# Performance work log

Measured on AMD Instinct MI355X. Metric: run time of the kernel, lower is better.

Reference implementation:

```python
import jax, jax.numpy as jnp
import numpy as np

HEAD = 16
EPS = 1.1920929e-07  # torch.finfo(float32).eps, used by nn.RMSNorm when eps=None


def _rms(x, g):
    return x * jax.lax.rsqrt(jnp.mean(x * x, axis=-1, keepdims=True) + EPS) * g


def _heads(t):
    b, L, dm = t.shape
    return t.reshape(b, L, HEAD, dm // HEAD).transpose(0, 2, 1, 3)  # b h L d


def setup_inputs() -> dict:
    key = jax.random.key(0)
    ks = jax.random.split(key, 8)
    b, L, dims = 1, 1024, 1024
    s = dims ** -0.5
    x = jax.random.normal(ks[0], (b, L, dims), jnp.float32)
    pt = jax.random.normal(ks[1], (b, L, dims), jnp.float32)
    # additive causal mask (finite large-negative to stay grad-safe)
    mask = jnp.triu(jnp.full((L, L), -1e9, jnp.float32), k=1)
    return {
        "x": x, "pt": pt, "mask": mask,
        "gq": jnp.ones((dims,), jnp.float32),
        "Wq": jax.random.normal(ks[2], (dims, dims), jnp.float32) * s,
        "bq": jnp.zeros((dims,), jnp.float32),
        "gkv": jnp.ones((dims,), jnp.float32),
        "Wkv": jax.random.normal(ks[3], (dims, 2 * dims), jnp.float32) * s,
        "bkv": jnp.zeros((2 * dims,), jnp.float32),
        "gc": jnp.ones((dims,), jnp.float32),
        "Wc": jax.random.normal(ks[4], (dims, dims), jnp.float32) * s,
        "bc": jnp.zeros((dims,), jnp.float32),
        "Wout": jax.random.normal(ks[5], (dims, dims), jnp.float32) * s,
        "bout": jnp.zeros((dims,), jnp.float32),
        "context_window": 16,
    }


def reference(x, pt, mask, gq, Wq, bq, gkv, Wkv, bkv, gc, Wc, bc, Wout, bout, context_window):
    b, L, dims = x.shape
    d = dims // HEAD
    q = _heads(_rms(x, gq) @ Wq + bq)                      # b h L d
    kv = (_rms(x, gkv) @ Wkv + bkv).reshape(b, L, 2, HEAD, d)
    k = kv[:, :, 0].transpose(0, 2, 1, 3)                  # b h L d
    v = kv[:, :, 1].transpose(0, 2, 1, 3)
    c = _heads(_rms(pt, gc) @ Wc + bc)                     # b h L d

    # triplet_scores[i,j] = sum_{t=max(0,min(i,j)-w)}^{min(L,max(i,j)+w)-1} q_i . (k_j * c_t)
    # Vectorize with prefix sums over c: window sum = P[end] - P[start],
    # where end depends only on max(i,j) and start only on min(i,j).
    P = jnp.concatenate([jnp.zeros((b, HEAD, 1, d), x.dtype), jnp.cumsum(c, axis=2)], axis=2)  # b h L+1 d
    idx = jnp.arange(L)
    S = jnp.clip(idx - context_window, 0, L)   # start for min-index
    E = jnp.clip(idx + context_window, 0, L)   # end for max-index
    PE = jnp.take(P, E, axis=2)                # b h L d
    PS = jnp.take(P, S, axis=2)

    U = jnp.einsum('bhid,bhjd->bhij', q, k * PE)        # end from j (i<=j branch)
    V = jnp.einsum('bhid,bhjd->bhij', q * PS, k)        # start from i (i<=j branch)
    U2 = jnp.einsum('bhid,bhjd->bhij', q * PE, k)       # end from i (i>j branch)
    V2 = jnp.einsum('bhid,bhjd->bhij', q, k * PS)       # start from j (i>j branch)
    lower = idx[:, None] <= idx[None, :]
    triplet = jnp.where(lower, U - V, U2 - V2)          # b h L L

    scale = d ** -0.5
    qk = jnp.einsum('bhid,bhjd->bhij', q, k) * scale + triplet + mask[:L, :L]
    attn = jax.nn.softmax(qk, axis=-1)
    wv = jnp.einsum('bhij,bhjd->bhid', attn, v)
    out = wv.transpose(0, 2, 1, 3).reshape(b, L, dims) @ Wout + bout  # dropout p=0.01 is identity at eval
    return out
```

## Files before the change

kernel.cpp:

```cpp
#include <hip/hip_runtime.h>

#define LQ 1024
#define DM 1024


typedef __attribute__((ext_vector_type(8))) short bf16x8;
typedef __attribute__((ext_vector_type(4))) float f32x4;

#define MFMA(a, b, c) __builtin_amdgcn_mfma_f32_16x16x32_bf16((a), (b), (c), 0, 0, 0)
#define WAIT_LDS() __builtin_amdgcn_s_waitcnt(0xC07F)

__device__ __forceinline__ unsigned short f2bf(float x) {
    unsigned int u = __float_as_uint(x);
    return (unsigned short)((u + 0x7FFFu + ((u >> 16) & 1u)) >> 16);
}
__device__ __forceinline__ float bf2f(unsigned short h) {
    return __uint_as_float(((unsigned int)h) << 16);
}
__device__ __forceinline__ void gload16(const void* gp, void* lp) {
    __builtin_amdgcn_global_load_lds(
        (const __attribute__((address_space(1))) void*)gp,
        (__attribute__((address_space(3))) void*)lp, 16, 0, 0);
}
__device__ __forceinline__ void store_split4(unsigned short* ph, unsigned short* pl,
                                             float4 v) {
    unsigned short h0 = f2bf(v.x), h1 = f2bf(v.y), h2 = f2bf(v.z), h3 = f2bf(v.w);
    uint2 a;
    a.x = (unsigned)h0 | ((unsigned)h1 << 16);
    a.y = (unsigned)h2 | ((unsigned)h3 << 16);
    *(uint2*)ph = a;
    unsigned short l0 = f2bf(v.x - bf2f(h0)), l1 = f2bf(v.y - bf2f(h1));
    unsigned short l2 = f2bf(v.z - bf2f(h2)), l3 = f2bf(v.w - bf2f(h3));
    uint2 b;
    b.x = (unsigned)l0 | ((unsigned)l1 << 16);
    b.y = (unsigned)l2 | ((unsigned)l3 << 16);
    *(uint2*)pl = b;
}

__device__ __forceinline__ void rms_body(
    int row, const float* __restrict__ x, const float* __restrict__ pt,
    const float* __restrict__ gq, const float* __restrict__ gkv,
    const float* __restrict__ gc,
    unsigned short* xqn_h, unsigned short* xqn_l,
    unsigned short* xkvn_h, unsigned short* xkvn_l,
    unsigned short* ptn_h, unsigned short* ptn_l)
{
    const int t = threadIdx.x;
    const bool isx = row < LQ;
    const float* src = isx ? (x + (size_t)row * DM)
                           : (pt + (size_t)(row - LQ) * DM);
    float4 v = ((const float4*)src)[t];
    float ss = v.x*v.x + v.y*v.y + v.z*v.z + v.w*v.w;
    #pragma unroll
    for (int o = 32; o > 0; o >>= 1) ss += __shfl_down(ss, o);
    __shared__ float red[4];
    if ((t & 63) == 0) red[t >> 6] = ss;
    __syncthreads();
    const float r = rsqrtf((red[0] + red[1] + red[2] + red[3]) * (1.0f / DM)
                           + 1.1920929e-07f);
    const size_t base = (size_t)(isx ? row : row - LQ) * DM + t * 4;
    if (isx) {
        float4 g1 = ((const float4*)gq)[t];
        float4 g2 = ((const float4*)gkv)[t];
        float4 y1, y2;
        y1.x = v.x*r*g1.x; y1.y = v.y*r*g1.y; y1.z = v.z*r*g1.z; y1.w = v.w*r*g1.w;
        y2.x = v.x*r*g2.x; y2.y = v.y*r*g2.y; y2.z = v.z*r*g2.z; y2.w = v.w*r*g2.w;
        store_split4(xqn_h + base, xqn_l + base, y1);
        store_split4(xkvn_h + base, xkvn_l + base, y2);
    } else {
        float4 g = ((const float4*)gc)[t];
        float4 y;
        y.x = v.x*r*g.x; y.y = v.y*r*g.y; y.z = v.z*r*g.z; y.w = v.w*r*g.w;
        store_split4(ptn_h + base, ptn_l + base, y);
    }
}

__device__ __forceinline__ void wsplit_body(
    const float* __restrict__ in, unsigned short* oh, unsigned short* ol,
    int K, int N, int bx, int by)
{
    __shared__ float T[64 * 65];
    const int t = threadIdx.x;
    const int tx = t & 15, ty = t >> 4;
    const int c0 = bx * 64, r0 = by * 64;
    #pragma unroll
    for (int p = 0; p < 4; ++p) {
        int row = ty + p * 16;
        float4 v = *(const float4*)(in + (size_t)(r0 + row) * N + c0 + tx * 4);
        T[row * 65 + tx * 4 + 0] = v.x;
        T[row * 65 + tx * 4 + 1] = v.y;
        T[row * 65 + tx * 4 + 2] = v.z;
        T[row * 65 + tx * 4 + 3] = v.w;
    }
    __syncthreads();
    #pragma unroll
    for (int p = 0; p < 4; ++p) {
        int n = ty + p * 16;
        float4 w;
        w.x = T[(tx * 4 + 0) * 65 + n];
        w.y = T[(tx * 4 + 1) * 65 + n];
        w.z = T[(tx * 4 + 2) * 65 + n];
        w.w = T[(tx * 4 + 3) * 65 + n];
        size_t o = (size_t)(c0 + n) * K + r0 + tx * 4;
        store_split4(oh + o, ol + o, w);
    }
}

__global__ __launch_bounds__(256) void prep_kernel(
    const float* __restrict__ x, const float* __restrict__ pt,
    const float* __restrict__ gq, const float* __restrict__ gkv,
    const float* __restrict__ gc,
    const float* __restrict__ Wq, const float* __restrict__ Wkv,
    const float* __restrict__ Wc, const float* __restrict__ Wout,
    unsigned short* xqn_h, unsigned short* xqn_l,
    unsigned short* xkvn_h, unsigned short* xkvn_l,
    unsigned short* ptn_h, unsigned short* ptn_l,
    unsigned short* WqT_h, unsigned short* WqT_l,
    unsigned short* WkvT_h, unsigned short* WkvT_l,
    unsigned short* WcT_h, unsigned short* WcT_l,
    unsigned short* WoT_h, unsigned short* WoT_l)
{
    const int b = blockIdx.x;
    if (b < 2048) {
        rms_body(b, x, pt, gq, gkv, gc, xqn_h, xqn_l, xkvn_h, xkvn_l, ptn_h, ptn_l);
    } else if (b < 2304) {
        int s = b - 2048; wsplit_body(Wq, WqT_h, WqT_l, 1024, 1024, s & 15, s >> 4);
    } else if (b < 2816) {
        int s = b - 2304; wsplit_body(Wkv, WkvT_h, WkvT_l, 1024, 2048, s & 31, s >> 5);
    } else if (b < 3072) {
        int s = b - 2816; wsplit_body(Wc, WcT_h, WcT_l, 1024, 1024, s & 15, s >> 4);
    } else {
        int s = b - 3072; wsplit_body(Wout, WoT_h, WoT_l, 1024, 1024, s & 15, s >> 4);
    }
}

__device__ __forceinline__ void gemm3p(
    const unsigned short* __restrict__ Ah, const unsigned short* __restrict__ Al,
    const unsigned short* __restrict__ Bh, const unsigned short* __restrict__ Bl,
    const float* __restrict__ bias, float* __restrict__ out, int N, int mt, int nt)
{
    __shared__ unsigned short sAh[128 * 32], sAl[128 * 32];
    __shared__ unsigned short sBh[64 * 32], sBl[64 * 32];
    const int t = threadIdx.x;
    const int lane = t & 63, w = t >> 6;
    const int wm = w >> 1, wn = w & 1;
    const int n16 = lane & 15, quad = lane >> 4;
    const int srow = t >> 2, scol = (t & 3) * 8;
    f32x4 zero = {0.f, 0.f, 0.f, 0.f};
    f32x4 acc[4][2];
    #pragma unroll
    for (int ms = 0; ms < 4; ++ms)
        #pragma unroll
        for (int ns = 0; ns < 2; ++ns) acc[ms][ns] = zero;

    for (int kt = 0; kt < 32; ++kt) {
        const int k0 = kt * 32;
        __syncthreads();
        #pragma unroll
        for (int p = 0; p < 2; ++p) {
            const size_t ga = (size_t)(mt * 128 + srow + p * 64) * 1024 + k0 + scol;
            const int lb = w * 512 + p * 2048;
            gload16(Ah + ga, sAh + lb);
            gload16(Al + ga, sAl + lb);
        }
        {
            const size_t gb = (size_t)(nt * 64 + srow) * 1024 + k0 + scol;
            gload16(Bh + gb, sBh + w * 512);
            gload16(Bl + gb, sBl + w * 512);
        }
        __syncthreads();
        bf16x8 afh[4], afl[4], bfh[2], bfl[2];
        #pragma unroll
        for (int ms = 0; ms < 4; ++ms) {
            int r = wm * 64 + ms * 16 + n16;
            afh[ms] = *(const bf16x8*)&sAh[r * 32 + quad * 8];
            afl[ms] = *(const bf16x8*)&sAl[r * 32 + quad * 8];
        }
        #pragma unroll
        for (int ns = 0; ns < 2; ++ns) {
            int r = wn * 32 + ns * 16 + n16;
            bfh[ns] = *(const bf16x8*)&sBh[r * 32 + quad * 8];
            bfl[ns] = *(const bf16x8*)&sBl[r * 32 + quad * 8];
        }
        #pragma unroll
        for (int ms = 0; ms < 4; ++ms)
            #pragma unroll
            for (int ns = 0; ns < 2; ++ns) {
                acc[ms][ns] = MFMA(afh[ms], bfh[ns], acc[ms][ns]);
                acc[ms][ns] = MFMA(afh[ms], bfl[ns], acc[ms][ns]);
                acc[ms][ns] = MFMA(afl[ms], bfh[ns], acc[ms][ns]);
            }
    }
    #pragma unroll
    for (int ns = 0; ns < 2; ++ns) {
        const int col = nt * 64 + wn * 32 + ns * 16 + n16;
        const float bv = bias[col];
        #pragma unroll
        for (int ms = 0; ms < 4; ++ms) {
            const int row0 = mt * 128 + wm * 64 + ms * 16 + quad * 4;
            #pragma unroll
            for (int reg = 0; reg < 4; ++reg)
                out[(size_t)(row0 + reg) * N + col] = acc[ms][ns][reg] + bv;
        }
    }
}

__global__ __launch_bounds__(256) void proj_kernel(
    const unsigned short* __restrict__ xqn_h, const unsigned short* __restrict__ xqn_l,
    const unsigned short* __restrict__ xkvn_h, const unsigned short* __restrict__ xkvn_l,
    const unsigned short* __restrict__ ptn_h, const unsigned short* __restrict__ ptn_l,
    const unsigned short* __restrict__ WqT_h, const unsigned short* __restrict__ WqT_l,
    const unsigned short* __restrict__ WkvT_h, const unsigned short* __restrict__ WkvT_l,
    const unsigned short* __restrict__ WcT_h, const unsigned short* __restrict__ WcT_l,
    const float* __restrict__ bq, const float* __restrict__ bkv,
    const float* __restrict__ bc,
    float* __restrict__ Qb, float* __restrict__ KVb, float* __restrict__ Cb)
{
    const int bid = blockIdx.x;
    if (bid < 128) {
        gemm3p(xqn_h, xqn_l, WqT_h, WqT_l, bq, Qb, 1024, bid >> 4, bid & 15);
    } else if (bid < 384) {
        int b2 = bid - 128;
        gemm3p(xkvn_h, xkvn_l, WkvT_h, WkvT_l, bkv, KVb, 2048, b2 >> 5, b2 & 31);
    } else {
        int b2 = bid - 384;
        gemm3p(ptn_h, ptn_l, WcT_h, WcT_l, bc, Cb, 1024, b2 >> 4, b2 & 15);
    }
}

__global__ __launch_bounds__(256) void csum_kernel(const float* __restrict__ Cb,
                                                   float* __restrict__ csum)
{
    const int cid = blockIdx.x >> 2;
    const int col = ((blockIdx.x & 3) << 8) + threadIdx.x;
    const float* p = Cb + (size_t)cid * 32 * 1024 + col;
    float s = 0.f;
    #pragma unroll 8
    for (int r = 0; r < 32; ++r) s += p[(size_t)r * 1024];
    csum[cid * 1024 + col] = s;
}

__global__ __launch_bounds__(256) void scanp_kernel(const float* __restrict__ Cb,
                                                    const float* __restrict__ csum,
                                                    float* __restrict__ Pb)
{
    const int cid = blockIdx.x >> 2;
    const int col = ((blockIdx.x & 3) << 8) + threadIdx.x;
    float run = 0.f;
    for (int c = 0; c < cid; ++c) run += csum[c * 1024 + col];
    const float* p = Cb + (size_t)cid * 32 * 1024 + col;
    float* q = Pb + (size_t)cid * 32 * 1024 + col;
    for (int r = 0; r < 32; ++r) {
        q[(size_t)r * 1024] = run;
        run += p[(size_t)r * 1024];
    }
    if (cid == 31) Pb[(size_t)1024 * 1024 + col] = run;
}

__global__ __launch_bounds__(256) void abv_kernel(
    const float* __restrict__ Qb, const float* __restrict__ KVb,
    const float* __restrict__ Pb, const int* __restrict__ cwp,
    unsigned short* __restrict__ Aah, unsigned short* __restrict__ Aal,
    unsigned short* __restrict__ Bah, unsigned short* __restrict__ Bal,
    unsigned short* __restrict__ VT)
{
    const int b = blockIdx.x;
    if (b < 4096) {
        const int gid = b * 256 + threadIdx.x;
        const int i = gid >> 10;
        const int col = gid & 1023;
        const int h = col >> 6, dd = col & 63;
        const int cw = *cwp;
        const int E = min(i + cw, LQ);
        const int S = max(i - cw, 0);
        const float pe = Pb[(size_t)E * 1024 + col];
        const float ps = Pb[(size_t)S * 1024 + col];
        const float q = Qb[gid];
        const float k = KVb[(size_t)i * 2048 + col];
        const float scale = 0.125f;
        const size_t base = ((size_t)(h * 1024 + i)) * 128;
        float a0 = q, a1 = q * pe;
        float b0 = k * (scale - ps), b1 = k;
        unsigned short hv;
        hv = f2bf(a0); Aah[base + dd] = hv;      Aal[base + dd] = f2bf(a0 - bf2f(hv));
        hv = f2bf(a1); Aah[base + 64 + dd] = hv; Aal[base + 64 + dd] = f2bf(a1 - bf2f(hv));
        hv = f2bf(b0); Bah[base + dd] = hv;      Bal[base + dd] = f2bf(b0 - bf2f(hv));
        hv = f2bf(b1); Bah[base + 64 + dd] = hv; Bal[base + 64 + dd] = f2bf(b1 - bf2f(hv));
    } else {
        const int s = b - 4096;
        const int h = s >> 4, j0 = (s & 15) * 64;
        __shared__ float T[64 * 65];
        const int t = threadIdx.x;
        const int tx = t & 15, ty = t >> 4;
        #pragma unroll
        for (int p = 0; p < 4; ++p) {
            int j = ty + p * 16;
            float4 v = *(const float4*)(KVb + (size_t)(j0 + j) * 2048 + 1024 + h * 64 + tx * 4);
            T[j * 65 + tx * 4 + 0] = v.x;
            T[j * 65 + tx * 4 + 1] = v.y;
            T[j * 65 + tx * 4 + 2] = v.z;
            T[j * 65 + tx * 4 + 3] = v.w;
        }
        __syncthreads();
        #pragma unroll
        for (int p = 0; p < 4; ++p) {
            int d = ty + p * 16;
            unsigned short e0 = f2bf(T[(tx * 4 + 0) * 65 + d]);
            unsigned short e1 = f2bf(T[(tx * 4 + 1) * 65 + d]);
            unsigned short e2 = f2bf(T[(tx * 4 + 2) * 65 + d]);
            unsigned short e3 = f2bf(T[(tx * 4 + 3) * 65 + d]);
            uint2 pk;
            pk.x = (unsigned)e0 | ((unsigned)e1 << 16);
            pk.y = (unsigned)e2 | ((unsigned)e3 << 16);
            *(uint2*)(VT + (size_t)(h * 64 + d) * 1024 + j0 + tx * 4) = pk;
        }
    }
}

__global__ __launch_bounds__(256, 4) void attn_kernel(
    const unsigned short* __restrict__ Aah, const unsigned short* __restrict__ Aal,
    const unsigned short* __restrict__ Bah, const unsigned short* __restrict__ Bal,
    const unsigned short* __restrict__ VT,
    unsigned short* __restrict__ wvh, unsigned short* __restrict__ wvl)
{
    __shared__ unsigned short PsAll[4][16 * 68];
    __shared__ float cO[4][16 * 68];
    __shared__ float cM[4][16], cL[4][16];

    const int t = threadIdx.x;
    const int lane = t & 63, wid = t >> 6;
    unsigned short* Ps = PsAll[wid];
    const int b = blockIdx.x;
    const int h = b & 15;
    const int q = (b >> 4) & 15;
    const int group = b >> 8;
    const int it16 = (group == 0) ? q : (group == 1) ? (31 - q)
                   : (group == 2) ? (32 + q) : (63 - q);
    const int i0 = it16 * 16;
    const int njt = (i0 >> 6) + 1;
    const int n16 = lane & 15, quad = lane >> 4;

    bf16x8 afh[4], afl[4];
    {
        const size_t ar = ((size_t)(h * 1024 + i0 + n16)) * 128 + quad * 8;
        #pragma unroll
        for (int kc = 0; kc < 4; ++kc) {
            afh[kc] = *(const bf16x8*)(Aah + ar + kc * 32);
            afl[kc] = *(const bf16x8*)(Aal + ar + kc * 32);
        }
    }

    f32x4 zero = {0.f, 0.f, 0.f, 0.f};
    f32x4 oacc[4];
    #pragma unroll
    for (int dt = 0; dt < 4; ++dt) oacc[dt] = zero;
    float mrow[4], lrow[4];
    #pragma unroll
    for (int reg = 0; reg < 4; ++reg) { mrow[reg] = -1e30f; lrow[reg] = 0.f; }

    for (int jt = wid; jt < njt; jt += 4) {
        const int j0 = jt * 64;
        f32x4 s[4];
        #pragma unroll
        for (int jj = 0; jj < 4; ++jj) s[jj] = zero;
        #pragma unroll
        for (int jj = 0; jj < 4; ++jj) {
            const size_t br = ((size_t)(h * 1024 + j0 + jj * 16 + n16)) * 128 + quad * 8;
            #pragma unroll
            for (int kc = 0; kc < 4; ++kc) {
                bf16x8 bh = *(const bf16x8*)(Bah + br + kc * 32);
                bf16x8 bl = *(const bf16x8*)(Bal + br + kc * 32);
                s[jj] = MFMA(afh[kc], bh, s[jj]);
                s[jj] = MFMA(afh[kc], bl, s[jj]);
                s[jj] = MFMA(afl[kc], bh, s[jj]);
            }
        }
        if (jt == njt - 1) {
            const int ibase = i0 + quad * 4;
            #pragma unroll
            for (int jj = 0; jj < 4; ++jj) {
                const int j = j0 + jj * 16 + n16;
                #pragma unroll
                for (int reg = 0; reg < 4; ++reg)
                    if (j > ibase + reg) s[jj][reg] = -1e30f;
            }
        }

        float alpha[4];
        #pragma unroll
        for (int reg = 0; reg < 4; ++reg) {
            float mt_ = fmaxf(fmaxf(s[0][reg], s[1][reg]), fmaxf(s[2][reg], s[3][reg]));
            mt_ = fmaxf(mt_, __shfl_xor(mt_, 1));
            mt_ = fmaxf(mt_, __shfl_xor(mt_, 2));
            mt_ = fmaxf(mt_, __shfl_xor(mt_, 4));
            mt_ = fmaxf(mt_, __shfl_xor(mt_, 8));
            const float mn = fmaxf(mrow[reg], mt_);
            alpha[reg] = __expf(mrow[reg] - mn);
            mrow[reg] = mn;
            float rs = 0.f;
            #pragma unroll
            for (int jj = 0; jj < 4; ++jj) {
                float p = __expf(s[jj][reg] - mn);
                s[jj][reg] = p;
                rs += p;
            }
            rs += __shfl_xor(rs, 1); rs += __shfl_xor(rs, 2);
            rs += __shfl_xor(rs, 4); rs += __shfl_xor(rs, 8);
            lrow[reg] = lrow[reg] * alpha[reg] + rs;
        }

        WAIT_LDS();
        #pragma unroll
        for (int jj = 0; jj < 4; ++jj)
            #pragma unroll
            for (int reg = 0; reg < 4; ++reg)
                Ps[(quad * 4 + reg) * 68 + jj * 16 + n16] = f2bf(s[jj][reg]);
        WAIT_LDS();
        bf16x8 pf0 = *(const bf16x8*)&Ps[n16 * 68 + quad * 8];
        bf16x8 pf1 = *(const bf16x8*)&Ps[n16 * 68 + 32 + quad * 8];

        #pragma unroll
        for (int dt = 0; dt < 4; ++dt) {
            #pragma unroll
            for (int reg = 0; reg < 4; ++reg) oacc[dt][reg] *= alpha[reg];
            const size_t vr = ((size_t)(h * 64 + dt * 16 + n16)) * 1024 + j0 + quad * 8;
            bf16x8 vf0 = *(const bf16x8*)(VT + vr);
            bf16x8 vf1 = *(const bf16x8*)(VT + vr + 32);
            oacc[dt] = MFMA(pf0, vf0, oacc[dt]);
            oacc[dt] = MFMA(pf1, vf1, oacc[dt]);
        }
    }

    #pragma unroll
    for (int dt = 0; dt < 4; ++dt)
        #pragma unroll
        for (int reg = 0; reg < 4; ++reg)
            cO[wid][(quad * 4 + reg) * 68 + dt * 16 + n16] = oacc[dt][reg];
    if (n16 == 0) {
        #pragma unroll
        for (int reg = 0; reg < 4; ++reg) {
            cM[wid][quad * 4 + reg] = mrow[reg];
            cL[wid][quad * 4 + reg] = lrow[reg];
        }
    }
    __syncthreads();
    #pragma unroll
    for (int u = 0; u < 4; ++u) {
        const int p = u * 256 + t;
        const int r = p >> 6, d = p & 63;
        const float m0 = cM[0][r], m1 = cM[1][r], m2 = cM[2][r], m3 = cM[3][r];
        const float M = fmaxf(fmaxf(m0, m1), fmaxf(m2, m3));
        const float e0 = __expf(m0 - M), e1 = __expf(m1 - M);
        const float e2 = __expf(m2 - M), e3 = __expf(m3 - M);
        const float L = e0 * cL[0][r] + e1 * cL[1][r] + e2 * cL[2][r] + e3 * cL[3][r];
        const float o = e0 * cO[0][r * 68 + d] + e1 * cO[1][r * 68 + d]
                      + e2 * cO[2][r * 68 + d] + e3 * cO[3][r * 68 + d];
        const float v = o / L;
        const size_t oi = (size_t)(i0 + r) * 1024 + h * 64 + d;
        const unsigned short hv = f2bf(v);
        wvh[oi] = hv;
        wvl[oi] = f2bf(v - bf2f(hv));
    }
}

__global__ __launch_bounds__(128) void outgemm_kernel(
    const unsigned short* __restrict__ Ah, const unsigned short* __restrict__ Al,
    const unsigned short* __restrict__ Bh, const unsigned short* __restrict__ Bl,
    const float* __restrict__ bias, float* __restrict__ out)
{
    __shared__ unsigned short sAh[64 * 32], sAl[64 * 32];
    __shared__ unsigned short sBh[32 * 32], sBl[32 * 32];
    const int t = threadIdx.x;
    const int lane = t & 63, w = t >> 6;
    const int n16 = lane & 15, quad = lane >> 4;
    const int mt = blockIdx.x >> 5, nt = blockIdx.x & 31;
    const int srow = t >> 2, scol = (t & 3) * 8;
    f32x4 zero = {0.f, 0.f, 0.f, 0.f};
    f32x4 acc[2][2];
    #pragma unroll
    for (int ms = 0; ms < 2; ++ms)
        #pragma unroll
        for (int ns = 0; ns < 2; ++ns) acc[ms][ns] = zero;

    for (int kt = 0; kt < 32; ++kt) {
        const int k0 = kt * 32;
        __syncthreads();
        #pragma unroll
        for (int p = 0; p < 2; ++p) {
            const size_t ga = (size_t)(mt * 64 + srow + p * 32) * 1024 + k0 + scol;
            const int lb = w * 512 + p * 1024;
            gload16(Ah + ga, sAh + lb);
            gload16(Al + ga, sAl + lb);
        }
        {
            const size_t gb = (size_t)(nt * 32 + srow) * 1024 + k0 + scol;
            gload16(Bh + gb, sBh + w * 512);
            gload16(Bl + gb, sBl + w * 512);
        }
        __syncthreads();
        bf16x8 ah[2], al[2], bh[2], bl[2];
        #pragma unroll
        for (int ms = 0; ms < 2; ++ms) {
            int r = w * 32 + ms * 16 + n16;
            ah[ms] = *(const bf16x8*)&sAh[r * 32 + quad * 8];
            al[ms] = *(const bf16x8*)&sAl[r * 32 + quad * 8];
        }
        #pragma unroll
        for (int ns = 0; ns < 2; ++ns) {
            int r = ns * 16 + n16;
            bh[ns] = *(const bf16x8*)&sBh[r * 32 + quad * 8];
            bl[ns] = *(const bf16x8*)&sBl[r * 32 + quad * 8];
        }
        #pragma unroll
        for (int ms = 0; ms < 2; ++ms)
            #pragma unroll
            for (int ns = 0; ns < 2; ++ns) {
                acc[ms][ns] = MFMA(ah[ms], bh[ns], acc[ms][ns]);
                acc[ms][ns] = MFMA(ah[ms], bl[ns], acc[ms][ns]);
                acc[ms][ns] = MFMA(al[ms], bh[ns], acc[ms][ns]);
            }
    }
    #pragma unroll
    for (int ns = 0; ns < 2; ++ns) {
        const int col = nt * 32 + ns * 16 + n16;
        const float bv = bias[col];
        #pragma unroll
        for (int ms = 0; ms < 2; ++ms) {
            const int row0 = mt * 64 + w * 32 + ms * 16 + quad * 4;
            #pragma unroll
            for (int reg = 0; reg < 4; ++reg)
                out[(size_t)(row0 + reg) * 1024 + col] = acc[ms][ns][reg] + bv;
        }
    }
}

extern "C" void kernel_launch(void* const* d_in, const int* in_sizes, int n_in,
                              void* d_out, int out_size, void* d_ws, size_t ws_size,
                              hipStream_t stream) {
    (void)in_sizes; (void)n_in; (void)out_size; (void)ws_size;
    const float* x    = (const float*)d_in[0];
    const float* pt   = (const float*)d_in[1];
    const float* gq   = (const float*)d_in[3];
    const float* Wq   = (const float*)d_in[4];
    const float* bq   = (const float*)d_in[5];
    const float* gkv  = (const float*)d_in[6];
    const float* Wkv  = (const float*)d_in[7];
    const float* bkv  = (const float*)d_in[8];
    const float* gc   = (const float*)d_in[9];
    const float* Wc   = (const float*)d_in[10];
    const float* bc   = (const float*)d_in[11];
    const float* Wout = (const float*)d_in[12];
    const float* bout = (const float*)d_in[13];
    const int*   cw   = (const int*)d_in[14];
    float* out = (float*)d_out;

    char* W = (char*)d_ws;
    const size_t MB = 1u << 20;
    #define US(off) ((unsigned short*)(W + (size_t)(off)))
    #define FP(off) ((float*)(W + (size_t)(off)))
    unsigned short* xqn_h  = US(0 * MB);
    unsigned short* xqn_l  = US(2 * MB);
    unsigned short* xkvn_h = US(4 * MB);
    unsigned short* xkvn_l = US(6 * MB);
    unsigned short* ptn_h  = US(8 * MB);
    unsigned short* ptn_l  = US(10 * MB);
    unsigned short* WqT_h  = US(12 * MB);
    unsigned short* WqT_l  = US(14 * MB);
    unsigned short* WkvT_h = US(16 * MB);
    unsigned short* WkvT_l = US(20 * MB);
    unsigned short* WcT_h  = US(24 * MB);
    unsigned short* WcT_l  = US(26 * MB);
    unsigned short* WoT_h  = US(28 * MB);
    unsigned short* WoT_l  = US(30 * MB);
    float* Qb   = FP(32 * MB);
    float* KVb  = FP(36 * MB);
    float* Cb   = FP(44 * MB);
    float* Pb   = FP(48 * MB);
    float* csum = FP(52 * MB + 256 * 1024);
    unsigned short* Aah = US(0 * MB);
    unsigned short* Aal = US(4 * MB);
    unsigned short* Bah = US(8 * MB);
    unsigned short* Bal = US(12 * MB);
    unsigned short* VTb = US(16 * MB);
    unsigned short* wv_h = US(18 * MB);
    unsigned short* wv_l = US(20 * MB);
    #undef US
    #undef FP

    hipLaunchKernelGGL(prep_kernel, dim3(3328), dim3(256), 0, stream,
                       x, pt, gq, gkv, gc, Wq, Wkv, Wc, Wout,
                       xqn_h, xqn_l, xkvn_h, xkvn_l, ptn_h, ptn_l,
                       WqT_h, WqT_l, WkvT_h, WkvT_l, WcT_h, WcT_l, WoT_h, WoT_l);
    hipLaunchKernelGGL(proj_kernel, dim3(512), dim3(256), 0, stream,
                       xqn_h, xqn_l, xkvn_h, xkvn_l, ptn_h, ptn_l,
                       WqT_h, WqT_l, WkvT_h, WkvT_l, WcT_h, WcT_l,
                       bq, bkv, bc, Qb, KVb, Cb);
    hipLaunchKernelGGL(csum_kernel, dim3(128), dim3(256), 0, stream, Cb, csum);
    hipLaunchKernelGGL(scanp_kernel, dim3(128), dim3(256), 0, stream, Cb, csum, Pb);
    hipLaunchKernelGGL(abv_kernel, dim3(4352), dim3(256), 0, stream,
                       Qb, KVb, Pb, cw, Aah, Aal, Bah, Bal, VTb);
    hipLaunchKernelGGL(attn_kernel, dim3(1024), dim3(256), 0, stream,
                       Aah, Aal, Bah, Bal, VTb, wv_h, wv_l);
    hipLaunchKernelGGL(outgemm_kernel, dim3(512), dim3(128), 0, stream,
                       wv_h, wv_l, WoT_h, WoT_l, bout, out);
}
```

Baseline: 225.3 us.

## Process two 16-row query tiles per 512-thread attention block, prefetch V earlier

The attention kernel now uses 512-thread blocks that each cover 32 query rows: pairs of waves share a key tile index, with each wave of a pair handling one 16-row half. Because the two halves read the same K/V tiles, those tiles can be reused through cache. The grid halves to 512 blocks, and block ordering pairs early and late rows to balance causal work. V fragments are now loaded right after the score MFMAs so their latency overlaps the softmax. The final combine reduces over the four waves belonging to each half. In exchange, register pressure and LDS use per block go up, and the coarser blocks could reduce occupancy or load balance.

New measurement: 239.2 us. 6.2% more time.

```diff
diff --git a/kernel.cpp b/kernel.cpp
--- a/kernel.cpp
+++ b/kernel.cpp
@@ -317,27 +317,27 @@
     }
 }
 
-__global__ __launch_bounds__(256, 4) void attn_kernel(
+__global__ __launch_bounds__(512, 4) void attn_kernel(
     const unsigned short* __restrict__ Aah, const unsigned short* __restrict__ Aal,
     const unsigned short* __restrict__ Bah, const unsigned short* __restrict__ Bal,
     const unsigned short* __restrict__ VT,
     unsigned short* __restrict__ wvh, unsigned short* __restrict__ wvl)
 {
-    __shared__ unsigned short PsAll[4][16 * 68];
-    __shared__ float cO[4][16 * 68];
-    __shared__ float cM[4][16], cL[4][16];
+    __shared__ unsigned short PsAll[8][16 * 68];
+    __shared__ float cO[8][16 * 68];
+    __shared__ float cM[8][16], cL[8][16];
 
     const int t = threadIdx.x;
     const int lane = t & 63, wid = t >> 6;
+    const int jp = wid >> 1, isub = wid & 1;
     unsigned short* Ps = PsAll[wid];
     const int b = blockIdx.x;
     const int h = b & 15;
-    const int q = (b >> 4) & 15;
-    const int group = b >> 8;
-    const int it16 = (group == 0) ? q : (group == 1) ? (31 - q)
-                   : (group == 2) ? (32 + q) : (63 - q);
-    const int i0 = it16 * 16;
-    const int njt = (i0 >> 6) + 1;
+    const int q4 = (b >> 4) & 15;
+    const int it32 = (b >> 8) ? (31 - q4) : q4;
+    const int i0b = it32 * 32;
+    const int i0 = i0b + isub * 16;
+    const int njt = (it32 >> 1) + 1;
     const int n16 = lane & 15, quad = lane >> 4;
 
     bf16x8 afh[4], afl[4];
@@ -358,7 +358,7 @@
     #pragma unroll
     for (int reg = 0; reg < 4; ++reg) { mrow[reg] = -1e30f; lrow[reg] = 0.f; }
 
-    for (int jt = wid; jt < njt; jt += 4) {
+    for (int jt = jp; jt < njt; jt += 4) {
         const int j0 = jt * 64;
         f32x4 s[4];
         #pragma unroll
@@ -375,6 +375,15 @@
                 s[jj] = MFMA(afl[kc], bh, s[jj]);
             }
         }
+
+        bf16x8 vf[4][2];
+        #pragma unroll
+        for (int dt = 0; dt < 4; ++dt) {
+            const size_t vr = ((size_t)(h * 64 + dt * 16 + n16)) * 1024 + j0 + quad * 8;
+            vf[dt][0] = *(const bf16x8*)(VT + vr);
+            vf[dt][1] = *(const bf16x8*)(VT + vr + 32);
+        }
+
         if (jt == njt - 1) {
             const int ibase = i0 + quad * 4;
             #pragma unroll
@@ -423,11 +432,8 @@
         for (int dt = 0; dt < 4; ++dt) {
             #pragma unroll
             for (int reg = 0; reg < 4; ++reg) oacc[dt][reg] *= alpha[reg];
-            const size_t vr = ((size_t)(h * 64 + dt * 16 + n16)) * 1024 + j0 + quad * 8;
-            bf16x8 vf0 = *(const bf16x8*)(VT + vr);
-            bf16x8 vf1 = *(const bf16x8*)(VT + vr + 32);
-            oacc[dt] = MFMA(pf0, vf0, oacc[dt]);
-            oacc[dt] = MFMA(pf1, vf1, oacc[dt]);
+            oacc[dt] = MFMA(pf0, vf[dt][0], oacc[dt]);
+            oacc[dt] = MFMA(pf1, vf[dt][1], oacc[dt]);
         }
     }
 
@@ -446,17 +452,20 @@
     __syncthreads();
     #pragma unroll
     for (int u = 0; u < 4; ++u) {
-        const int p = u * 256 + t;
-        const int r = p >> 6, d = p & 63;
-        const float m0 = cM[0][r], m1 = cM[1][r], m2 = cM[2][r], m3 = cM[3][r];
+        const int p = u * 512 + t;
+        const int s = p >> 10;
+        const int rem = p & 1023;
+        const int r = rem >> 6, d = rem & 63;
+        const int w0 = s, w1 = s + 2, w2 = s + 4, w3 = s + 6;
+        const float m0 = cM[w0][r], m1 = cM[w1][r], m2 = cM[w2][r], m3 = cM[w3][r];
         const float M = fmaxf(fmaxf(m0, m1), fmaxf(m2, m3));
         const float e0 = __expf(m0 - M), e1 = __expf(m1 - M);
         const float e2 = __expf(m2 - M), e3 = __expf(m3 - M);
-        const float L = e0 * cL[0][r] + e1 * cL[1][r] + e2 * cL[2][r] + e3 * cL[3][r];
-        const float o = e0 * cO[0][r * 68 + d] + e1 * cO[1][r * 68 + d]
-                      + e2 * cO[2][r * 68 + d] + e3 * cO[3][r * 68 + d];
+        const float L = e0 * cL[w0][r] + e1 * cL[w1][r] + e2 * cL[w2][r] + e3 * cL[w3][r];
+        const float o = e0 * cO[w0][r * 68 + d] + e1 * cO[w1][r * 68 + d]
+                      + e2 * cO[w2][r * 68 + d] + e3 * cO[w3][r * 68 + d];
         const float v = o / L;
-        const size_t oi = (size_t)(i0 + r) * 1024 + h * 64 + d;
+        const size_t oi = (size_t)(i0b + s * 16 + r) * 1024 + h * 64 + d;
         const unsigned short hv = f2bf(v);
         wvh[oi] = hv;
         wvl[oi] = f2bf(v - bf2f(hv));
@@ -599,7 +608,7 @@
     hipLaunchKernelGGL(scanp_kernel, dim3(128), dim3(256), 0, stream, Cb, csum, Pb);
     hipLaunchKernelGGL(abv_kernel, dim3(4352), dim3(256), 0, stream,
                        Qb, KVb, Pb, cw, Aah, Aal, Bah, Bal, VTb);
-    hipLaunchKernelGGL(attn_kernel, dim3(1024), dim3(256), 0, stream,
+    hipLaunchKernelGGL(attn_kernel, dim3(512), dim3(512), 0, stream,
                        Aah, Aal, Bah, Bal, VTb, wv_h, wv_l);
     hipLaunchKernelGGL(outgemm_kernel, dim3(512), dim3(128), 0, stream,
                        wv_h, wv_l, WoT_h, WoT_l, bout, out);
```

## Enlarge GEMM tiles to 128x128 and 64x64, reload Q fragments per tile

Applied to the files above, without the earlier changes.

The projection GEMM moves from 128x64 tiles with 256 threads to 128x128 tiles with 512 threads (8 waves as 2x4). The output GEMM moves from 64x32 tiles with 128 threads to 64x64 tiles with 256 threads (2x2 waves). Both halve the grid and cut redundant global loads of the shared operand. The attention kernel now loads the A fragments inside the j-tile loop instead of once before it, which lowers register pressure but adds repeated global reads. The larger blocks also mean fewer blocks in flight on the device.

Measured after the change: 234.2 us. 1.04x slower.

```diff
diff --git a/kernel.cpp b/kernel.cpp
--- a/kernel.cpp
+++ b/kernel.cpp
@@ -140,10 +140,10 @@
     const float* __restrict__ bias, float* __restrict__ out, int N, int mt, int nt)
 {
     __shared__ unsigned short sAh[128 * 32], sAl[128 * 32];
-    __shared__ unsigned short sBh[64 * 32], sBl[64 * 32];
+    __shared__ unsigned short sBh[128 * 32], sBl[128 * 32];
     const int t = threadIdx.x;
     const int lane = t & 63, w = t >> 6;
-    const int wm = w >> 1, wn = w & 1;
+    const int wm = w >> 2, wn = w & 3;
     const int n16 = lane & 15, quad = lane >> 4;
     const int srow = t >> 2, scol = (t & 3) * 8;
     f32x4 zero = {0.f, 0.f, 0.f, 0.f};
@@ -155,19 +155,13 @@
 
     for (int kt = 0; kt < 32; ++kt) {
         const int k0 = kt * 32;
+        const size_t ga = (size_t)(mt * 128 + srow) * 1024 + k0 + scol;
+        const size_t gb = (size_t)(nt * 128 + srow) * 1024 + k0 + scol;
         __syncthreads();
-        #pragma unroll
-        for (int p = 0; p < 2; ++p) {
-            const size_t ga = (size_t)(mt * 128 + srow + p * 64) * 1024 + k0 + scol;
-            const int lb = w * 512 + p * 2048;
-            gload16(Ah + ga, sAh + lb);
-            gload16(Al + ga, sAl + lb);
-        }
-        {
-            const size_t gb = (size_t)(nt * 64 + srow) * 1024 + k0 + scol;
-            gload16(Bh + gb, sBh + w * 512);
-            gload16(Bl + gb, sBl + w * 512);
-        }
+        gload16(Ah + ga, sAh + w * 512);
+        gload16(Al + ga, sAl + w * 512);
+        gload16(Bh + gb, sBh + w * 512);
+        gload16(Bl + gb, sBl + w * 512);
         __syncthreads();
         bf16x8 afh[4], afl[4], bfh[2], bfl[2];
         #pragma unroll
@@ -193,7 +187,7 @@
     }
     #pragma unroll
     for (int ns = 0; ns < 2; ++ns) {
-        const int col = nt * 64 + wn * 32 + ns * 16 + n16;
+        const int col = nt * 128 + wn * 32 + ns * 16 + n16;
         const float bv = bias[col];
         #pragma unroll
         for (int ms = 0; ms < 4; ++ms) {
@@ -205,7 +199,7 @@
     }
 }
 
-__global__ __launch_bounds__(256) void proj_kernel(
+__global__ __launch_bounds__(512) void proj_kernel(
     const unsigned short* __restrict__ xqn_h, const unsigned short* __restrict__ xqn_l,
     const unsigned short* __restrict__ xkvn_h, const unsigned short* __restrict__ xkvn_l,
     const unsigned short* __restrict__ ptn_h, const unsigned short* __restrict__ ptn_l,
@@ -217,14 +211,14 @@
     float* __restrict__ Qb, float* __restrict__ KVb, float* __restrict__ Cb)
 {
     const int bid = blockIdx.x;
-    if (bid < 128) {
-        gemm3p(xqn_h, xqn_l, WqT_h, WqT_l, bq, Qb, 1024, bid >> 4, bid & 15);
-    } else if (bid < 384) {
-        int b2 = bid - 128;
-        gemm3p(xkvn_h, xkvn_l, WkvT_h, WkvT_l, bkv, KVb, 2048, b2 >> 5, b2 & 31);
+    if (bid < 64) {
+        gemm3p(xqn_h, xqn_l, WqT_h, WqT_l, bq, Qb, 1024, bid >> 3, bid & 7);
+    } else if (bid < 192) {
+        int b2 = bid - 64;
+        gemm3p(xkvn_h, xkvn_l, WkvT_h, WkvT_l, bkv, KVb, 2048, b2 >> 4, b2 & 15);
     } else {
-        int b2 = bid - 384;
-        gemm3p(ptn_h, ptn_l, WcT_h, WcT_l, bc, Cb, 1024, b2 >> 4, b2 & 15);
+        int b2 = bid - 192;
+        gemm3p(ptn_h, ptn_l, WcT_h, WcT_l, bc, Cb, 1024, b2 >> 3, b2 & 7);
     }
 }
 
@@ -340,26 +334,24 @@
     const int njt = (i0 >> 6) + 1;
     const int n16 = lane & 15, quad = lane >> 4;
 
-    bf16x8 afh[4], afl[4];
-    {
-        const size_t ar = ((size_t)(h * 1024 + i0 + n16)) * 128 + quad * 8;
+    f32x4 zero = {0.f, 0.f, 0.f, 0.f};
+    f32x4 oacc[4];
+    #pragma unroll
+    for (int dt = 0; dt < 4; ++dt) oacc[dt] = zero;
+    float mrow[4], lrow[4];
+    #pragma unroll
+    for (int reg = 0; reg < 4; ++reg) { mrow[reg] = -1e30f; lrow[reg] = 0.f; }
+
+    const size_t ar = ((size_t)(h * 1024 + i0 + n16)) * 128 + quad * 8;
+
+    for (int jt = wid; jt < njt; jt += 4) {
+        const int j0 = jt * 64;
+        bf16x8 afh[4], afl[4];
         #pragma unroll
         for (int kc = 0; kc < 4; ++kc) {
             afh[kc] = *(const bf16x8*)(Aah + ar + kc * 32);
             afl[kc] = *(const bf16x8*)(Aal + ar + kc * 32);
         }
-    }
-
-    f32x4 zero = {0.f, 0.f, 0.f, 0.f};
-    f32x4 oacc[4];
-    #pragma unroll
-    for (int dt = 0; dt < 4; ++dt) oacc[dt] = zero;
-    float mrow[4], lrow[4];
-    #pragma unroll
-    for (int reg = 0; reg < 4; ++reg) { mrow[reg] = -1e30f; lrow[reg] = 0.f; }
-
-    for (int jt = wid; jt < njt; jt += 4) {
-        const int j0 = jt * 64;
         f32x4 s[4];
         #pragma unroll
         for (int jj = 0; jj < 4; ++jj) s[jj] = zero;
@@ -463,17 +455,18 @@
     }
 }
 
-__global__ __launch_bounds__(128) void outgemm_kernel(
+__global__ __launch_bounds__(256) void outgemm_kernel(
     const unsigned short* __restrict__ Ah, const unsigned short* __restrict__ Al,
     const unsigned short* __restrict__ Bh, const unsigned short* __restrict__ Bl,
     const float* __restrict__ bias, float* __restrict__ out)
 {
     __shared__ unsigned short sAh[64 * 32], sAl[64 * 32];
-    __shared__ unsigned short sBh[32 * 32], sBl[32 * 32];
+    __shared__ unsigned short sBh[64 * 32], sBl[64 * 32];
     const int t = threadIdx.x;
     const int lane = t & 63, w = t >> 6;
+    const int wm = w >> 1, wn = w & 1;
     const int n16 = lane & 15, quad = lane >> 4;
-    const int mt = blockIdx.x >> 5, nt = blockIdx.x & 31;
+    const int mt = blockIdx.x >> 4, nt = blockIdx.x & 15;
     const int srow = t >> 2, scol = (t & 3) * 8;
     f32x4 zero = {0.f, 0.f, 0.f, 0.f};
     f32x4 acc[2][2];
@@ -484,30 +477,24 @@
 
     for (int kt = 0; kt < 32; ++kt) {
         const int k0 = kt * 32;
+        const size_t ga = (size_t)(mt * 64 + srow) * 1024 + k0 + scol;
+        const size_t gb = (size_t)(nt * 64 + srow) * 1024 + k0 + scol;
         __syncthreads();
-        #pragma unroll
-        for (int p = 0; p < 2; ++p) {
-            const size_t ga = (size_t)(mt * 64 + srow + p * 32) * 1024 + k0 + scol;
-            const int lb = w * 512 + p * 1024;
-            gload16(Ah + ga, sAh + lb);
-            gload16(Al + ga, sAl + lb);
-        }
-        {
-            const size_t gb = (size_t)(nt * 32 + srow) * 1024 + k0 + scol;
-            gload16(Bh + gb, sBh + w * 512);
-            gload16(Bl + gb, sBl + w * 512);
-        }
+        gload16(Ah + ga, sAh + w * 512);
+        gload16(Al + ga, sAl + w * 512);
+        gload16(Bh + gb, sBh + w * 512);
+        gload16(Bl + gb, sBl + w * 512);
         __syncthreads();
         bf16x8 ah[2], al[2], bh[2], bl[2];
         #pragma unroll
         for (int ms = 0; ms < 2; ++ms) {
-            int r = w * 32 + ms * 16 + n16;
+            int r = wm * 32 + ms * 16 + n16;
             ah[ms] = *(const bf16x8*)&sAh[r * 32 + quad * 8];
             al[ms] = *(const bf16x8*)&sAl[r * 32 + quad * 8];
         }
         #pragma unroll
         for (int ns = 0; ns < 2; ++ns) {
-            int r = ns * 16 + n16;
+            int r = wn * 32 + ns * 16 + n16;
             bh[ns] = *(const bf16x8*)&sBh[r * 32 + quad * 8];
             bl[ns] = *(const bf16x8*)&sBl[r * 32 + quad * 8];
         }
@@ -522,11 +509,11 @@
     }
     #pragma unroll
     for (int ns = 0; ns < 2; ++ns) {
-        const int col = nt * 32 + ns * 16 + n16;
+        const int col = nt * 64 + wn * 32 + ns * 16 + n16;
         const float bv = bias[col];
         #pragma unroll
         for (int ms = 0; ms < 2; ++ms) {
-            const int row0 = mt * 64 + w * 32 + ms * 16 + quad * 4;
+            const int row0 = mt * 64 + wm * 32 + ms * 16 + quad * 4;
             #pragma unroll
             for (int reg = 0; reg < 4; ++reg)
                 out[(size_t)(row0 + reg) * 1024 + col] = acc[ms][ns][reg] + bv;
@@ -591,7 +578,7 @@
                        x, pt, gq, gkv, gc, Wq, Wkv, Wc, Wout,
                        xqn_h, xqn_l, xkvn_h, xkvn_l, ptn_h, ptn_l,
                        WqT_h, WqT_l, WkvT_h, WkvT_l, WcT_h, WcT_l, WoT_h, WoT_l);
-    hipLaunchKernelGGL(proj_kernel, dim3(512), dim3(256), 0, stream,
+    hipLaunchKernelGGL(proj_kernel, dim3(256), dim3(512), 0, stream,
                        xqn_h, xqn_l, xkvn_h, xkvn_l, ptn_h, ptn_l,
                        WqT_h, WqT_l, WkvT_h, WkvT_l, WcT_h, WcT_l,
                        bq, bkv, bc, Qb, KVb, Cb);
@@ -601,6 +588,6 @@
                        Qb, KVb, Pb, cw, Aah, Aal, Bah, Bal, VTb);
     hipLaunchKernelGGL(attn_kernel, dim3(1024), dim3(256), 0, stream,
                        Aah, Aal, Bah, Bal, VTb, wv_h, wv_l);
-    hipLaunchKernelGGL(outgemm_kernel, dim3(512), dim3(128), 0, stream,
+    hipLaunchKernelGGL(outgemm_kernel, dim3(256), dim3(256), 0, stream,
                        wv_h, wv_l, WoT_h, WoT_l, bout, out);
 }
```
